# Kernel optimization log

Measured on AMD Instinct MI355X. Metric: run time of the kernel, lower is better.

## Reference

```python
import jax, jax.numpy as jnp
import numpy as np

SIZE = 1024
CODE_DIM = 256
N = 65536

def setup_inputs() -> dict:
    key = jax.random.key(0)
    k1, k2 = jax.random.split(key)
    z = jax.random.normal(k1, (N, CODE_DIM), dtype=jnp.float32)
    # nn.Embedding weight initialized uniform(-1/size, 1/size)
    weight = jax.random.uniform(k2, (SIZE, CODE_DIM), dtype=jnp.float32,
                                minval=-1.0 / SIZE, maxval=1.0 / SIZE)
    return {"z": z, "weight": weight}

def reference(z, weight):
    flat = z.reshape(-1, CODE_DIM)                       # [N, D]
    distances = (jnp.sum(flat ** 2, axis=1, keepdims=True)
                 - 2.0 * flat @ weight.T
                 + jnp.sum(weight ** 2, axis=1)[None, :])  # [N, SIZE]
    encoding_indices = jnp.argmax(-distances, axis=1)     # [N]
    quantized = weight[encoding_indices]                  # [N, D]
    return quantized, encoding_indices
```

## Files before the change

kernel.cpp:

```cpp
#include <hip/hip_runtime.h>
#include <hip/hip_bf16.h>
#include <stdint.h>
#include <float.h>


constexpr int NROWS = 65536;
constexpr int D     = 256;
constexpr int CODES = 1024;

constexpr float TAU_SCREEN = 2.5e-4f;
constexpr int   MAXPAIRS   = 7000000;

typedef __attribute__((ext_vector_type(8))) short short8;
typedef __attribute__((ext_vector_type(4))) float f32x4;

__device__ __forceinline__ void gl2lds16(const unsigned short* g, unsigned short* l) {
    __builtin_amdgcn_global_load_lds(
        (const __attribute__((address_space(1))) void*)g,
        (__attribute__((address_space(3))) void*)l, 16, 0, 0);
}

__device__ __forceinline__ unsigned short f2bf(float x) {
    union { __hip_bfloat16 h; unsigned short u; } c;
    c.h = __float2bfloat16(x);
    return c.u;
}

__device__ __forceinline__ void cvt8(const float* __restrict__ src,
                                     unsigned short* __restrict__ dst, int i) {
    const float4* s = (const float4*)src + (size_t)i * 2;
    float4 a = s[0], b = s[1];
    union { unsigned short u[8]; uint4 v; } p;
    p.u[0] = f2bf(a.x); p.u[1] = f2bf(a.y); p.u[2] = f2bf(a.z); p.u[3] = f2bf(a.w);
    p.u[4] = f2bf(b.x); p.u[5] = f2bf(b.y); p.u[6] = f2bf(b.z); p.u[7] = f2bf(b.w);
    *(uint4*)(dst + (size_t)i * 8) = p.v;
}

__global__ __launch_bounds__(256) void vq_prep(const float* __restrict__ z,
                                               unsigned short* __restrict__ zbf,
                                               const float* __restrict__ w,
                                               unsigned short* __restrict__ wbf,
                                               float* __restrict__ Cn,
                                               int* __restrict__ cnt,
                                               int* __restrict__ pcnt,
                                               unsigned long long* __restrict__ packed) {
    const int b = blockIdx.x;
    const int t = threadIdx.x;
    if (b < 8192) {
        cvt8(z, zbf, b * 256 + t);
    } else if (b < 8320) {
        cvt8(w, wbf, (b - 8192) * 256 + t);
    } else if (b < 8324) {
        const int row = (b - 8320) * 256 + t;
        const float4* p = (const float4*)(w + (size_t)row * D);
        float res[2];
        #pragma unroll
        for (int h = 0; h < 2; ++h) {
            float r[8];
            #pragma unroll
            for (int j = 0; j < 8; ++j) r[j] = 0.f;
            #pragma unroll 4
            for (int mm = 0; mm < 16; ++mm) {
                const float4 v0 = p[h * 32 + mm * 2];
                const float4 v1 = p[h * 32 + mm * 2 + 1];
                r[0] = __fadd_rn(r[0], __fmul_rn(v0.x, v0.x));
                r[1] = __fadd_rn(r[1], __fmul_rn(v0.y, v0.y));
                r[2] = __fadd_rn(r[2], __fmul_rn(v0.z, v0.z));
                r[3] = __fadd_rn(r[3], __fmul_rn(v0.w, v0.w));
                r[4] = __fadd_rn(r[4], __fmul_rn(v1.x, v1.x));
                r[5] = __fadd_rn(r[5], __fmul_rn(v1.y, v1.y));
                r[6] = __fadd_rn(r[6], __fmul_rn(v1.z, v1.z));
                r[7] = __fadd_rn(r[7], __fmul_rn(v1.w, v1.w));
            }
            res[h] = __fadd_rn(__fadd_rn(__fadd_rn(r[0], r[1]), __fadd_rn(r[2], r[3])),
                               __fadd_rn(__fadd_rn(r[4], r[5]), __fadd_rn(r[6], r[7])));
        }
        Cn[row] = __fadd_rn(res[0], res[1]);
    } else {
        const int i = (b - 8324) * 256 + t;
        packed[i] = ~0ull;
        if (i == 0) { *cnt = 0; *pcnt = 0; }
    }
}

__global__ __launch_bounds__(512, 4) void vq_screen(const unsigned short* __restrict__ zbf,
                                                    const unsigned short* __restrict__ wbf,
                                                    const float* __restrict__ Cn,
                                                    int* __restrict__ idx_out,
                                                    int* __restrict__ flagged,
                                                    int* __restrict__ cnt,
                                                    float* __restrict__ m1_out) {
    __shared__ unsigned short zT[2][128 * 64];
    __shared__ unsigned short wT[2][128 * 64];
    __shared__ float Cs[1024];
    __shared__ float rm1s[2][128];
    __shared__ float rm2s[2][128];
    __shared__ int   ris[2][128];

    const int t    = threadIdx.x;
    const int wv   = t >> 6;
    const int l    = t & 63;
    const int wm   = wv >> 1;
    const int wn   = wv & 1;
    const int m    = l & 15;
    const int quad = l >> 4;
    const int row0 = blockIdx.x * 128;

    const int  srow8   = l >> 3;
    const int  schunk  = (l & 7) ^ srow8;
    const size_t laneoff = (size_t)srow8 * D + schunk * 8;

    for (int i = t; i < 1024; i += 512) Cs[i] = Cn[i];

    float m1[2][4], m2[2][4];
    int   bi[2][4];
    f32x4 acc[2][4];
    #pragma unroll
    for (int mi = 0; mi < 2; ++mi)
        #pragma unroll
        for (int r = 0; r < 4; ++r) {
            m1[mi][r] = FLT_MAX; m2[mi][r] = FLT_MAX; bi[mi][r] = 0;
            acc[mi][r] = (f32x4){0.f, 0.f, 0.f, 0.f};
        }

    #define STAGE(s_, buf_) do {                                                    \
        const int nb_ = (s_) >> 2, ks_ = (s_) & 3;                                  \
        _Pragma("unroll")                                                           \
        for (int i_ = 0; i_ < 4; ++i_) {                                            \
            const int u_ = wv * 4 + i_;                                             \
            if (u_ < 16)                                                            \
                gl2lds16(zbf + (size_t)(row0 + u_ * 8) * D + ks_ * 64 + laneoff,    \
                         &zT[buf_][u_ * 512]);                                      \
            else                                                                    \
                gl2lds16(wbf + (size_t)(nb_ * 128 + (u_ - 16) * 8) * D + ks_ * 64   \
                             + laneoff,                                             \
                         &wT[buf_][(u_ - 16) * 512]);                               \
        }                                                                           \
    } while (0)

    STAGE(0, 0);

    #pragma unroll 2
    for (int s = 0; s < 32; ++s) {
        const int cur = s & 1;
        if (s < 31) {
            STAGE(s + 1, cur ^ 1);
            asm volatile("s_waitcnt vmcnt(4) lgkmcnt(0)" ::: "memory");
        } else {
            asm volatile("s_waitcnt vmcnt(0) lgkmcnt(0)" ::: "memory");
        }
        asm volatile("s_barrier" ::: "memory");

        #pragma unroll
        for (int kk = 0; kk < 2; ++kk) {
            short8 a[2], b[4];
            const int ch = kk * 4 + quad;
            const int co = (ch ^ (m & 7)) * 8;
            #pragma unroll
            for (int mi = 0; mi < 2; ++mi)
                a[mi] = *(const short8*)&zT[cur][(wm * 32 + mi * 16 + m) * 64 + co];
            #pragma unroll
            for (int ni = 0; ni < 4; ++ni)
                b[ni] = *(const short8*)&wT[cur][(wn * 64 + ni * 16 + m) * 64 + co];
            #pragma unroll
            for (int mi = 0; mi < 2; ++mi)
                #pragma unroll
                for (int ni = 0; ni < 4; ++ni)
                    acc[mi][ni] = __builtin_amdgcn_mfma_f32_16x16x32_bf16(
                        a[mi], b[ni], acc[mi][ni], 0, 0, 0);
        }
        asm volatile("s_barrier" ::: "memory");

        if ((s & 3) == 3) {
            const int nb = s >> 2;
            #pragma unroll
            for (int ni = 0; ni < 4; ++ni) {
                const int code = nb * 128 + wn * 64 + ni * 16 + m;
                const float c  = Cs[code];
                #pragma unroll
                for (int mi = 0; mi < 2; ++mi)
                    #pragma unroll
                    for (int r = 0; r < 4; ++r) {
                        const float v  = fmaf(-2.0f, acc[mi][ni][r], c);
                        const float o1 = m1[mi][r];
                        bi[mi][r] = (v < o1) ? code : bi[mi][r];
                        m2[mi][r] = __builtin_amdgcn_fmed3f(o1, m2[mi][r], v);
                        m1[mi][r] = fminf(o1, v);
                        acc[mi][ni][r] = 0.f;
                    }
            }
        }
    }
    #undef STAGE

    #pragma unroll
    for (int mi = 0; mi < 2; ++mi)
        #pragma unroll
        for (int r = 0; r < 4; ++r) {
            float a1 = m1[mi][r], a2 = m2[mi][r];
            int   ai = bi[mi][r];
            #pragma unroll
            for (int off = 1; off <= 8; off <<= 1) {
                const float o1 = __shfl_xor(a1, off, 64);
                const float o2 = __shfl_xor(a2, off, 64);
                const int   oi = __shfl_xor(ai, off, 64);
                const float n1 = fminf(a1, o1);
                const float n2 = fminf(fminf(a2, o2), fmaxf(a1, o1));
                ai = (o1 < a1) ? oi : ai;
                a1 = n1; a2 = n2;
            }
            m1[mi][r] = a1; m2[mi][r] = a2; bi[mi][r] = ai;
        }

    if (m == 0) {
        #pragma unroll
        for (int mi = 0; mi < 2; ++mi)
            #pragma unroll
            for (int r = 0; r < 4; ++r) {
                const int rl = wm * 32 + mi * 16 + quad * 4 + r;
                rm1s[wn][rl] = m1[mi][r];
                rm2s[wn][rl] = m2[mi][r];
                ris[wn][rl]  = bi[mi][r];
            }
    }
    __syncthreads();
    if (t < 128) {
        float a1 = rm1s[0][t], a2 = rm2s[0][t];
        int   ai = ris[0][t];
        const float o1 = rm1s[1][t], o2 = rm2s[1][t];
        const int   oi = ris[1][t];
        const float n1 = fminf(a1, o1);
        const float n2 = fminf(fminf(a2, o2), fmaxf(a1, o1));
        ai = (o1 < a1) ? oi : ai;
        a1 = n1; a2 = n2;
        const int row = row0 + t;
        idx_out[row] = ai;
        m1_out[row]  = a1;
        if (a2 - a1 < TAU_SCREEN) {
            int p = atomicAdd(cnt, 1);
            flagged[p] = row;
        }
    }
}

__global__ __launch_bounds__(256, 2) void vq_cand(const unsigned short* __restrict__ zbf,
                                                  const unsigned short* __restrict__ wbf,
                                                  const float* __restrict__ Cn,
                                                  const float* __restrict__ m1g,
                                                  const int* __restrict__ flagged,
                                                  const int* __restrict__ cnt,
                                                  uint32_t* __restrict__ pairs,
                                                  int* __restrict__ pcnt) {
    __shared__ union SM {
        struct { unsigned short zT[2][128 * 64]; unsigned short wT[2][128 * 64]; } tl;
        uint32_t list[16384];
    } sm;
    __shared__ int rows_s[128];
    __shared__ int lcnt;
    __shared__ int gbase;

    const int t    = threadIdx.x;
    const int wv   = t >> 6;
    const int l    = t & 63;
    const int wm   = wv >> 1;
    const int wn   = wv & 1;
    const int m    = l & 15;
    const int quad = l >> 4;

    const int  srow8   = l >> 3;
    const int  schunk  = (l & 7) ^ srow8;
    const size_t laneoff_w = (size_t)srow8 * D + schunk * 8;
    const bool stz   = (wv < 2);
    const int  sbase = (wv & 1) * 64;

    const int n     = *cnt;
    const int njobs = ((n + 127) >> 7) << 3;

    for (int job = blockIdx.x; job < njobs; job += gridDim.x) {
        const int tile = job >> 3;
        const int nb   = job & 7;
        __syncthreads();
        if (t < 128) {
            const int fi = tile * 128 + t;
            rows_s[t] = (fi < n) ? flagged[fi] : -1;
        }
        if (t == 0) lcnt = 0;
        __syncthreads();

        int zrow[8];
        #pragma unroll
        for (int i = 0; i < 8; ++i) {
            const int rr = rows_s[sbase + i * 8 + srow8];
            zrow[i] = rr < 0 ? 0 : rr;
        }
        int   rowid[4][4];
        float thr[4][4];
        #pragma unroll
        for (int mi = 0; mi < 4; ++mi)
            #pragma unroll
            for (int r = 0; r < 4; ++r) {
                const int rl = wm * 64 + mi * 16 + quad * 4 + r;
                const int ri = rows_s[rl];
                rowid[mi][r] = ri;
                thr[mi][r]   = (ri >= 0) ? m1g[ri] + TAU_SCREEN : -FLT_MAX;
            }

        f32x4 acc[4][4];
        #pragma unroll
        for (int mi = 0; mi < 4; ++mi)
            #pragma unroll
            for (int ni = 0; ni < 4; ++ni) acc[mi][ni] = (f32x4){0.f, 0.f, 0.f, 0.f};

        #define STAGEC(ks_, buf_) do {                                                \
            if (stz) {                                                                \
                unsigned short* ldsb_ = &sm.tl.zT[buf_][sbase * 64];                  \
                _Pragma("unroll")                                                     \
                for (int i_ = 0; i_ < 8; ++i_)                                        \
                    gl2lds16(zbf + (size_t)zrow[i_] * D + (ks_) * 64 + schunk * 8,    \
                             ldsb_ + i_ * 512);                                       \
            } else {                                                                  \
                unsigned short* ldsb_ = &sm.tl.wT[buf_][sbase * 64];                  \
                const unsigned short* gb_ =                                           \
                    wbf + (size_t)(nb * 128 + sbase) * D + (ks_) * 64;                \
                _Pragma("unroll")                                                     \
                for (int i_ = 0; i_ < 8; ++i_)                                        \
                    gl2lds16(gb_ + (size_t)i_ * 8 * D + laneoff_w, ldsb_ + i_ * 512); \
            }                                                                         \
        } while (0)

        STAGEC(0, 0);
        for (int ks = 0; ks < 4; ++ks) {
            const int cur = ks & 1;
            if (ks < 3) {
                STAGEC(ks + 1, cur ^ 1);
                asm volatile("s_waitcnt vmcnt(8) lgkmcnt(0)" ::: "memory");
            } else {
                asm volatile("s_waitcnt vmcnt(0) lgkmcnt(0)" ::: "memory");
            }
            asm volatile("s_barrier" ::: "memory");
            #pragma unroll
            for (int kk = 0; kk < 2; ++kk) {
                short8 a[4], b[4];
                const int ch = kk * 4 + quad;
                const int co = (ch ^ (m & 7)) * 8;
                #pragma unroll
                for (int mi = 0; mi < 4; ++mi)
                    a[mi] = *(const short8*)&sm.tl.zT[cur][(wm * 64 + mi * 16 + m) * 64 + co];
                #pragma unroll
                for (int ni = 0; ni < 4; ++ni)
                    b[ni] = *(const short8*)&sm.tl.wT[cur][(wn * 64 + ni * 16 + m) * 64 + co];
                #pragma unroll
                for (int mi = 0; mi < 4; ++mi)
                    #pragma unroll
                    for (int ni = 0; ni < 4; ++ni)
                        acc[mi][ni] = __builtin_amdgcn_mfma_f32_16x16x32_bf16(
                            a[mi], b[ni], acc[mi][ni], 0, 0, 0);
            }
            asm volatile("s_barrier" ::: "memory");
        }
        #undef STAGEC

        #pragma unroll
        for (int ni = 0; ni < 4; ++ni) {
            const int code = nb * 128 + wn * 64 + ni * 16 + m;
            const float c  = Cn[code];
            #pragma unroll
            for (int mi = 0; mi < 4; ++mi)
                #pragma unroll
                for (int r = 0; r < 4; ++r) {
                    const float v = fmaf(-2.0f, acc[mi][ni][r], c);
                    if (v < thr[mi][r]) {
                        const int p = atomicAdd(&lcnt, 1);
                        sm.list[p] = ((uint32_t)rowid[mi][r] << 16) | (uint32_t)code;
                    }
                }
        }
        __syncthreads();
        if (t == 0) gbase = atomicAdd(pcnt, lcnt);
        __syncthreads();
        const int nc = lcnt;
        const int gb = gbase;
        for (int i = t; i < nc; i += 256) {
            const int p = gb + i;
            if (p < MAXPAIRS) pairs[p] = sm.list[i];
        }
    }
}

__global__ __launch_bounds__(256) void vq_exact(const float* __restrict__ z,
                                                const float* __restrict__ w,
                                                const float* __restrict__ Cn,
                                                const uint32_t* __restrict__ pairs,
                                                const int* __restrict__ pcnt,
                                                unsigned long long* __restrict__ packed) {
    const int np0 = *pcnt;
    const int np  = np0 < MAXPAIRS ? np0 : MAXPAIRS;
    for (int g = blockIdx.x * 256 + threadIdx.x; g < np; g += gridDim.x * 256) {
        const uint32_t pr = pairs[g];
        const int row  = (int)(pr >> 16);
        const int code = (int)(pr & 0xffffu);
        const float4* zp = (const float4*)(z + (size_t)row * D);
        const float4* wp = (const float4*)(w + (size_t)code * D);
        float B = 0.f;
        float res[2];
        #pragma unroll
        for (int b = 0; b < 2; ++b) {
            float r[8];
            #pragma unroll
            for (int j = 0; j < 8; ++j) r[j] = 0.f;
            #pragma unroll 4
            for (int mm = 0; mm < 16; ++mm) {
                const float4 z0 = zp[b * 32 + mm * 2];
                const float4 z1 = zp[b * 32 + mm * 2 + 1];
                const float4 w0 = wp[b * 32 + mm * 2];
                const float4 w1 = wp[b * 32 + mm * 2 + 1];
                r[0] = __fadd_rn(r[0], __fmul_rn(z0.x, z0.x));
                r[1] = __fadd_rn(r[1], __fmul_rn(z0.y, z0.y));
                r[2] = __fadd_rn(r[2], __fmul_rn(z0.z, z0.z));
                r[3] = __fadd_rn(r[3], __fmul_rn(z0.w, z0.w));
                r[4] = __fadd_rn(r[4], __fmul_rn(z1.x, z1.x));
                r[5] = __fadd_rn(r[5], __fmul_rn(z1.y, z1.y));
                r[6] = __fadd_rn(r[6], __fmul_rn(z1.z, z1.z));
                r[7] = __fadd_rn(r[7], __fmul_rn(z1.w, z1.w));
                B = fmaf(z0.x, w0.x, B); B = fmaf(z0.y, w0.y, B);
                B = fmaf(z0.z, w0.z, B); B = fmaf(z0.w, w0.w, B);
                B = fmaf(z1.x, w1.x, B); B = fmaf(z1.y, w1.y, B);
                B = fmaf(z1.z, w1.z, B); B = fmaf(z1.w, w1.w, B);
            }
            res[b] = __fadd_rn(__fadd_rn(__fadd_rn(r[0], r[1]), __fadd_rn(r[2], r[3])),
                               __fadd_rn(__fadd_rn(r[4], r[5]), __fadd_rn(r[6], r[7])));
        }
        const float A = __fadd_rn(res[0], res[1]);
        const float d = __fadd_rn(__fsub_rn(A, __fmul_rn(2.0f, B)), Cn[code]);
        const uint32_t bits = __float_as_uint(d);
        const uint32_t ord  = (bits & 0x80000000u) ? ~bits : (bits | 0x80000000u);
        const unsigned long long key =
            ((unsigned long long)ord << 32) | (unsigned long long)(uint32_t)code;
        atomicMin(&packed[row], key);
    }
}

__global__ __launch_bounds__(256) void vq_unpack(const int* __restrict__ flagged,
                                                 const int* __restrict__ cnt,
                                                 const unsigned long long* __restrict__ packed,
                                                 int* __restrict__ idx) {
    const int n = *cnt;
    for (int g = blockIdx.x * 256 + threadIdx.x; g < n; g += gridDim.x * 256) {
        const int row = flagged[g];
        idx[row] = (int)(packed[row] & 0xffffffffull);
    }
}

__global__ __launch_bounds__(256) void vq_gather(const float* __restrict__ w,
                                                 const int* __restrict__ idx,
                                                 float* __restrict__ outq,
                                                 float* __restrict__ outi) {
    const int t    = threadIdx.x;
    const int lane = t & 63;
    const int sub  = t >> 6;
    const int row0 = blockIdx.x * 128;
    #pragma unroll 4
    for (int it = 0; it < 32; ++it) {
        const int row = row0 + it * 4 + sub;
        const int j   = idx[row];
        ((float4*)outq)[(size_t)row * 64 + lane] = ((const float4*)w)[(size_t)j * 64 + lane];
        if (lane == 0) outi[row] = (float)j;
    }
}

extern "C" void kernel_launch(void* const* d_in, const int* in_sizes, int n_in,
                              void* d_out, int out_size, void* d_ws, size_t ws_size,
                              hipStream_t stream) {
    const float* z = (const float*)d_in[0];
    const float* w = (const float*)d_in[1];
    float* outq = (float*)d_out;
    float* outi = outq + (size_t)NROWS * D;

    unsigned short*     zbf    = (unsigned short*)d_out;
    unsigned short*     wbf    = (unsigned short*)((char*)d_out + 33554432);
    float*              Cn     = (float*)((char*)d_out + 34078720);
    float*              m1g    = (float*)((char*)d_out + 36700160);
    unsigned long long* packed = (unsigned long long*)((char*)d_out + 37224448);
    uint32_t*           pairs  = (uint32_t*)((char*)d_out + 37748736);

    char* ws      = (char*)d_ws;
    int*  idx     = (int*)ws;
    int*  flagged = (int*)(ws + 262144);
    int*  cnt     = (int*)(ws + 524288);
    int*  pcnt    = (int*)(ws + 524292);

    vq_prep<<<8580, 256, 0, stream>>>(z, zbf, w, wbf, Cn, cnt, pcnt, packed);
    vq_screen<<<NROWS / 128, 512, 0, stream>>>(zbf, wbf, Cn, idx, flagged, cnt, m1g);
    vq_cand<<<512, 256, 0, stream>>>(zbf, wbf, Cn, m1g, flagged, cnt, pairs, pcnt);
    vq_exact<<<256, 256, 0, stream>>>(z, w, Cn, pairs, pcnt, packed);
    vq_unpack<<<64, 256, 0, stream>>>(flagged, cnt, packed, idx);
    vq_gather<<<NROWS / 128, 256, 0, stream>>>(w, idx, outq, outi);
}
```

Before: 222.4 us.

## Fuse z fp32-to-bf16 conversion into screen and candidate GEMM kernels

Drops the separate pass that converted all of z to bf16 in global memory. The screen and candidate kernels now load their fp32 z rows directly, convert them in registers and keep the full 128x256 bf16 tile resident in LDS for the whole K loop, so only the codebook tiles are streamed and double-buffered. This removes a 64MB read plus 32MB write-and-reread round trip. In exchange the LDS footprint per block grows (zT is now 64KB), which together with the dropped occupancy hint in launch_bounds may lower occupancy, and the z load happens serially before the GEMM loop starts.

```diff
diff --git a/kernel.cpp b/kernel.cpp
--- a/kernel.cpp
+++ b/kernel.cpp
@@ -26,19 +26,20 @@
     return c.u;
 }
 
+__device__ __forceinline__ uint4 pack8(float4 a, float4 b) {
+    union { unsigned short u[8]; uint4 v; } p;
+    p.u[0] = f2bf(a.x); p.u[1] = f2bf(a.y); p.u[2] = f2bf(a.z); p.u[3] = f2bf(a.w);
+    p.u[4] = f2bf(b.x); p.u[5] = f2bf(b.y); p.u[6] = f2bf(b.z); p.u[7] = f2bf(b.w);
+    return p.v;
+}
+
 __device__ __forceinline__ void cvt8(const float* __restrict__ src,
                                      unsigned short* __restrict__ dst, int i) {
     const float4* s = (const float4*)src + (size_t)i * 2;
-    float4 a = s[0], b = s[1];
-    union { unsigned short u[8]; uint4 v; } p;
-    p.u[0] = f2bf(a.x); p.u[1] = f2bf(a.y); p.u[2] = f2bf(a.z); p.u[3] = f2bf(a.w);
-    p.u[4] = f2bf(b.x); p.u[5] = f2bf(b.y); p.u[6] = f2bf(b.z); p.u[7] = f2bf(b.w);
-    *(uint4*)(dst + (size_t)i * 8) = p.v;
-}
-
-__global__ __launch_bounds__(256) void vq_prep(const float* __restrict__ z,
-                                               unsigned short* __restrict__ zbf,
-                                               const float* __restrict__ w,
+    *(uint4*)(dst + (size_t)i * 8) = pack8(s[0], s[1]);
+}
+
+__global__ __launch_bounds__(256) void vq_prep(const float* __restrict__ w,
                                                unsigned short* __restrict__ wbf,
                                                float* __restrict__ Cn,
                                                int* __restrict__ cnt,
@@ -46,12 +47,10 @@
                                                unsigned long long* __restrict__ packed) {
     const int b = blockIdx.x;
     const int t = threadIdx.x;
-    if (b < 8192) {
-        cvt8(z, zbf, b * 256 + t);
-    } else if (b < 8320) {
-        cvt8(w, wbf, (b - 8192) * 256 + t);
-    } else if (b < 8324) {
-        const int row = (b - 8320) * 256 + t;
+    if (b < 128) {
+        cvt8(w, wbf, b * 256 + t);
+    } else if (b < 132) {
+        const int row = (b - 128) * 256 + t;
         const float4* p = (const float4*)(w + (size_t)row * D);
         float res[2];
         #pragma unroll
@@ -77,20 +76,20 @@
         }
         Cn[row] = __fadd_rn(res[0], res[1]);
     } else {
-        const int i = (b - 8324) * 256 + t;
+        const int i = (b - 132) * 256 + t;
         packed[i] = ~0ull;
         if (i == 0) { *cnt = 0; *pcnt = 0; }
     }
 }
 
-__global__ __launch_bounds__(512, 4) void vq_screen(const unsigned short* __restrict__ zbf,
-                                                    const unsigned short* __restrict__ wbf,
-                                                    const float* __restrict__ Cn,
-                                                    int* __restrict__ idx_out,
-                                                    int* __restrict__ flagged,
-                                                    int* __restrict__ cnt,
-                                                    float* __restrict__ m1_out) {
-    __shared__ unsigned short zT[2][128 * 64];
+__global__ __launch_bounds__(512) void vq_screen(const float* __restrict__ z,
+                                                 const unsigned short* __restrict__ wbf,
+                                                 const float* __restrict__ Cn,
+                                                 int* __restrict__ idx_out,
+                                                 int* __restrict__ flagged,
+                                                 int* __restrict__ cnt,
+                                                 float* __restrict__ m1_out) {
+    __shared__ unsigned short zT[128 * 256];
     __shared__ unsigned short wT[2][128 * 64];
     __shared__ float Cs[1024];
     __shared__ float rm1s[2][128];
@@ -110,6 +109,14 @@
     const int  schunk  = (l & 7) ^ srow8;
     const size_t laneoff = (size_t)srow8 * D + schunk * 8;
 
+    #pragma unroll
+    for (int i = 0; i < 8; ++i) {
+        const int flat = i * 512 + t;
+        const int r    = flat >> 5;
+        const int gch  = flat & 31;
+        const float4* src = (const float4*)(z + (size_t)(row0 + r) * D + gch * 8);
+        *(uint4*)&zT[r * 256 + ((gch ^ (r & 7)) * 8)] = pack8(src[0], src[1]);
+    }
     for (int i = t; i < 1024; i += 512) Cs[i] = Cn[i];
 
     float m1[2][4], m2[2][4];
@@ -126,26 +133,22 @@
     #define STAGE(s_, buf_) do {                                                    \
         const int nb_ = (s_) >> 2, ks_ = (s_) & 3;                                  \
         _Pragma("unroll")                                                           \
-        for (int i_ = 0; i_ < 4; ++i_) {                                            \
-            const int u_ = wv * 4 + i_;                                             \
-            if (u_ < 16)                                                            \
-                gl2lds16(zbf + (size_t)(row0 + u_ * 8) * D + ks_ * 64 + laneoff,    \
-                         &zT[buf_][u_ * 512]);                                      \
-            else                                                                    \
-                gl2lds16(wbf + (size_t)(nb_ * 128 + (u_ - 16) * 8) * D + ks_ * 64   \
-                             + laneoff,                                             \
-                         &wT[buf_][(u_ - 16) * 512]);                               \
+        for (int i_ = 0; i_ < 2; ++i_) {                                            \
+            const int u_ = wv * 2 + i_;                                             \
+            gl2lds16(wbf + (size_t)(nb_ * 128 + u_ * 8) * D + ks_ * 64 + laneoff,   \
+                     &wT[buf_][u_ * 512]);                                          \
         }                                                                           \
     } while (0)
 
     STAGE(0, 0);
+    __syncthreads();
 
     #pragma unroll 2
     for (int s = 0; s < 32; ++s) {
         const int cur = s & 1;
         if (s < 31) {
             STAGE(s + 1, cur ^ 1);
-            asm volatile("s_waitcnt vmcnt(4) lgkmcnt(0)" ::: "memory");
+            asm volatile("s_waitcnt vmcnt(2) lgkmcnt(0)" ::: "memory");
         } else {
             asm volatile("s_waitcnt vmcnt(0) lgkmcnt(0)" ::: "memory");
         }
@@ -154,14 +157,16 @@
         #pragma unroll
         for (int kk = 0; kk < 2; ++kk) {
             short8 a[2], b[4];
-            const int ch = kk * 4 + quad;
-            const int co = (ch ^ (m & 7)) * 8;
+            const int ch   = kk * 4 + quad;
+            const int gchA = (s & 3) * 8 + ch;
+            const int coB  = (ch ^ (m & 7)) * 8;
             #pragma unroll
             for (int mi = 0; mi < 2; ++mi)
-                a[mi] = *(const short8*)&zT[cur][(wm * 32 + mi * 16 + m) * 64 + co];
+                a[mi] = *(const short8*)&zT[(wm * 32 + mi * 16 + m) * 256
+                                            + ((gchA ^ (m & 7)) * 8)];
             #pragma unroll
             for (int ni = 0; ni < 4; ++ni)
-                b[ni] = *(const short8*)&wT[cur][(wn * 64 + ni * 16 + m) * 64 + co];
+                b[ni] = *(const short8*)&wT[cur][(wn * 64 + ni * 16 + m) * 64 + coB];
             #pragma unroll
             for (int mi = 0; mi < 2; ++mi)
                 #pragma unroll
@@ -243,16 +248,16 @@
     }
 }
 
-__global__ __launch_bounds__(256, 2) void vq_cand(const unsigned short* __restrict__ zbf,
-                                                  const unsigned short* __restrict__ wbf,
-                                                  const float* __restrict__ Cn,
-                                                  const float* __restrict__ m1g,
-                                                  const int* __restrict__ flagged,
-                                                  const int* __restrict__ cnt,
-                                                  uint32_t* __restrict__ pairs,
-                                                  int* __restrict__ pcnt) {
+__global__ __launch_bounds__(256) void vq_cand(const float* __restrict__ z,
+                                               const unsigned short* __restrict__ wbf,
+                                               const float* __restrict__ Cn,
+                                               const float* __restrict__ m1g,
+                                               const int* __restrict__ flagged,
+                                               const int* __restrict__ cnt,
+                                               uint32_t* __restrict__ pairs,
+                                               int* __restrict__ pcnt) {
     __shared__ union SM {
-        struct { unsigned short zT[2][128 * 64]; unsigned short wT[2][128 * 64]; } tl;
+        struct { unsigned short zT[128 * 256]; unsigned short wT[2][128 * 64]; } tl;
         uint32_t list[16384];
     } sm;
     __shared__ int rows_s[128];
@@ -270,8 +275,6 @@
     const int  srow8   = l >> 3;
     const int  schunk  = (l & 7) ^ srow8;
     const size_t laneoff_w = (size_t)srow8 * D + schunk * 8;
-    const bool stz   = (wv < 2);
-    const int  sbase = (wv & 1) * 64;
 
     const int n     = *cnt;
     const int njobs = ((n + 127) >> 7) << 3;
@@ -287,12 +290,16 @@
         if (t == 0) lcnt = 0;
         __syncthreads();
 
-        int zrow[8];
-        #pragma unroll
-        for (int i = 0; i < 8; ++i) {
-            const int rr = rows_s[sbase + i * 8 + srow8];
-            zrow[i] = rr < 0 ? 0 : rr;
-        }
+        #pragma unroll
+        for (int i = 0; i < 16; ++i) {
+            const int flat = i * 256 + t;
+            const int r    = flat >> 5;
+            const int gch  = flat & 31;
+            const int rr   = rows_s[r] < 0 ? 0 : rows_s[r];
+            const float4* src = (const float4*)(z + (size_t)rr * D + gch * 8);
+            *(uint4*)&sm.tl.zT[r * 256 + ((gch ^ (r & 7)) * 8)] = pack8(src[0], src[1]);
+        }
+
         int   rowid[4][4];
         float thr[4][4];
         #pragma unroll
@@ -312,28 +319,23 @@
             for (int ni = 0; ni < 4; ++ni) acc[mi][ni] = (f32x4){0.f, 0.f, 0.f, 0.f};
 
         #define STAGEC(ks_, buf_) do {                                                \
-            if (stz) {                                                                \
-                unsigned short* ldsb_ = &sm.tl.zT[buf_][sbase * 64];                  \
-                _Pragma("unroll")                                                     \
-                for (int i_ = 0; i_ < 8; ++i_)                                        \
-                    gl2lds16(zbf + (size_t)zrow[i_] * D + (ks_) * 64 + schunk * 8,    \
-                             ldsb_ + i_ * 512);                                       \
-            } else {                                                                  \
-                unsigned short* ldsb_ = &sm.tl.wT[buf_][sbase * 64];                  \
-                const unsigned short* gb_ =                                           \
-                    wbf + (size_t)(nb * 128 + sbase) * D + (ks_) * 64;                \
-                _Pragma("unroll")                                                     \
-                for (int i_ = 0; i_ < 8; ++i_)                                        \
-                    gl2lds16(gb_ + (size_t)i_ * 8 * D + laneoff_w, ldsb_ + i_ * 512); \
+            _Pragma("unroll")                                                         \
+            for (int i_ = 0; i_ < 4; ++i_) {                                          \
+                const int u_ = wv * 4 + i_;                                           \
+                gl2lds16(wbf + (size_t)(nb * 128 + u_ * 8) * D + (ks_) * 64           \
+                             + laneoff_w,                                             \
+                         &sm.tl.wT[buf_][u_ * 512]);                                  \
             }                                                                         \
         } while (0)
 
         STAGEC(0, 0);
+        __syncthreads();
+
         for (int ks = 0; ks < 4; ++ks) {
             const int cur = ks & 1;
             if (ks < 3) {
                 STAGEC(ks + 1, cur ^ 1);
-                asm volatile("s_waitcnt vmcnt(8) lgkmcnt(0)" ::: "memory");
+                asm volatile("s_waitcnt vmcnt(4) lgkmcnt(0)" ::: "memory");
             } else {
                 asm volatile("s_waitcnt vmcnt(0) lgkmcnt(0)" ::: "memory");
             }
@@ -341,14 +343,16 @@
             #pragma unroll
             for (int kk = 0; kk < 2; ++kk) {
                 short8 a[4], b[4];
-                const int ch = kk * 4 + quad;
-                const int co = (ch ^ (m & 7)) * 8;
+                const int ch   = kk * 4 + quad;
+                const int gchA = ks * 8 + ch;
+                const int coB  = (ch ^ (m & 7)) * 8;
                 #pragma unroll
                 for (int mi = 0; mi < 4; ++mi)
-                    a[mi] = *(const short8*)&sm.tl.zT[cur][(wm * 64 + mi * 16 + m) * 64 + co];
+                    a[mi] = *(const short8*)&sm.tl.zT[(wm * 64 + mi * 16 + m) * 256
+                                                      + ((gchA ^ (m & 7)) * 8)];
                 #pragma unroll
                 for (int ni = 0; ni < 4; ++ni)
-                    b[ni] = *(const short8*)&sm.tl.wT[cur][(wn * 64 + ni * 16 + m) * 64 + co];
+                    b[ni] = *(const short8*)&sm.tl.wT[cur][(wn * 64 + ni * 16 + m) * 64 + coB];
                 #pragma unroll
                 for (int mi = 0; mi < 4; ++mi)
                     #pragma unroll
@@ -476,7 +480,6 @@
     float* outq = (float*)d_out;
     float* outi = outq + (size_t)NROWS * D;
 
-    unsigned short*     zbf    = (unsigned short*)d_out;
     unsigned short*     wbf    = (unsigned short*)((char*)d_out + 33554432);
     float*              Cn     = (float*)((char*)d_out + 34078720);
     float*              m1g    = (float*)((char*)d_out + 36700160);
@@ -489,9 +492,9 @@
     int*  cnt     = (int*)(ws + 524288);
     int*  pcnt    = (int*)(ws + 524292);
 
-    vq_prep<<<8580, 256, 0, stream>>>(z, zbf, w, wbf, Cn, cnt, pcnt, packed);
-    vq_screen<<<NROWS / 128, 512, 0, stream>>>(zbf, wbf, Cn, idx, flagged, cnt, m1g);
-    vq_cand<<<512, 256, 0, stream>>>(zbf, wbf, Cn, m1g, flagged, cnt, pairs, pcnt);
+    vq_prep<<<388, 256, 0, stream>>>(w, wbf, Cn, cnt, pcnt, packed);
+    vq_screen<<<NROWS / 128, 512, 0, stream>>>(z, wbf, Cn, idx, flagged, cnt, m1g);
+    vq_cand<<<512, 256, 0, stream>>>(z, wbf, Cn, m1g, flagged, cnt, pairs, pcnt);
     vq_exact<<<256, 256, 0, stream>>>(z, w, Cn, pairs, pcnt, packed);
     vq_unpack<<<64, 256, 0, stream>>>(flagged, cnt, packed, idx);
     vq_gather<<<NROWS / 128, 256, 0, stream>>>(w, idx, outq, outi);
```

Measured after the change: 224.6 us. About the same (+1.0%).
